# Kernel optimization log

Measured on AMD Instinct MI355X. Metric: run time of the kernel, lower is better.

## Reference

```python
import jax, jax.numpy as jnp
import numpy as np

TOP_K = 2
N_EXP = 64
EVAL_CAPACITY = 2.0


def setup_inputs() -> dict:
    key = jax.random.key(0)
    k1, k2 = jax.random.split(key)
    x = jax.random.normal(k1, (4, 4096, 2048), dtype=jnp.float32)
    w_g = jax.random.normal(k2, (N_EXP, 2048), dtype=jnp.float32) * 0.02  # Linear(n_embd, n_exp, bias=False)
    return {"x": x, "w_g": w_g}


def reference(x, w_g):
    B, T, C = x.shape
    num_tokens = B * T
    x_flat = x.reshape(num_tokens, C)
    # gating logits: [N, E]
    logits = jnp.einsum('nc,ec->ne', x_flat, w_g)
    # top-k selection
    top_k_logits, top_k_indices = jax.lax.top_k(logits, TOP_K)  # [N, k]
    router_probs = jax.nn.softmax(top_k_logits, axis=-1)        # [N, k]
    # static expert capacity (eval path)
    exp_capacity = max(int(TOP_K * EVAL_CAPACITY * num_tokens / N_EXP), 4)
    # one-hot expert mask [N, k, E]
    expert_mask = jax.nn.one_hot(top_k_indices, N_EXP, dtype=jnp.int32)
    # rank tokens within each expert via cumsum over (k-major, token) order
    reshaped = expert_mask.transpose(1, 0, 2).reshape(TOP_K * num_tokens, N_EXP)
    cumsum = jnp.cumsum(reshaped, axis=0)
    position = cumsum.reshape(TOP_K, num_tokens, N_EXP).transpose(1, 0, 2)  # [N, k, E]
    rank = (position - 1) * expert_mask
    capacity_mask = (rank < exp_capacity).astype(jnp.int32)
    final_mask = expert_mask * capacity_mask                     # [N, k, E]
    probs_mask = (final_mask.sum(axis=-1) > 0)                   # [N, k] bool
    router_probs_masked = router_probs * probs_mask.astype(router_probs.dtype)
    final_rank = rank.sum(axis=-1)                               # [N, k]
    return final_mask, router_probs_masked, top_k_indices, final_rank, exp_capacity
```

## Files before the change

kernel.cpp:

```cpp
#include <hip/hip_runtime.h>
#include <math.h>

#define C_DIM 2048
#define E_DIM 64
#define KC    128
#define BT    32
#define NW    4

typedef _Float16 h4    __attribute__((ext_vector_type(4)));
typedef _Float16 v8hf  __attribute__((ext_vector_type(8)));
typedef float    f32x4 __attribute__((ext_vector_type(4)));

#define SCALE      64.0f
#define INV_SCALE2 (1.0f/4096.0f)

__launch_bounds__(256)
__global__ void k_wsplit(const float* __restrict__ w, _Float16* __restrict__ wfrag)
{
    int t  = blockIdx.x * 256 + threadIdx.x;
    int l  = t & 63;
    int ni = (t >> 6) & 3;
    int q  = t >> 8;
    int e  = 16 * ni + (l & 15);
    int k0 = 32 * q + (l >> 4) * 8;
    const float* src = w + (size_t)e * C_DIM + k0;
    float4 a = *(const float4*)(src);
    float4 b = *(const float4*)(src + 4);
    float s[8] = {a.x, a.y, a.z, a.w, b.x, b.y, b.z, b.w};
    v8hf hv, lv;
#pragma unroll
    for (int j = 0; j < 8; ++j) {
        float sc = s[j] * SCALE;
        _Float16 h = (_Float16)sc;
        hv[j] = h;
        lv[j] = (_Float16)(sc - (float)h);
    }
    size_t fo = (size_t)(q * 4 + ni) * 1024;
    *(v8hf*)(wfrag + fo + l * 8)       = hv;
    *(v8hf*)(wfrag + fo + 512 + l * 8) = lv;
}

__launch_bounds__(256)
__global__ void k_logits_top2(const float* __restrict__ x, const _Float16* __restrict__ wfrag,
                              unsigned char* __restrict__ idx0, unsigned char* __restrict__ idx1,
                              float* __restrict__ dlt, unsigned short* __restrict__ gcounts,
                              int nblk)
{
    __shared__ alignas(16) char smem[2 * 16384];

    const int tid  = threadIdx.x;
    const int lane = tid & 63;
    const int wk   = tid >> 6;
    const int ln15 = lane & 15;
    const int g    = lane >> 4;
    const int t0   = blockIdx.x * BT;

    f32x4 acc[2][4];
#pragma unroll
    for (int mi = 0; mi < 2; ++mi)
#pragma unroll
        for (int ni = 0; ni < 4; ++ni) acc[mi][ni] = (f32x4)0.0f;

    float4 xr[4];
    v8hf bh[2][4], bl[2][4];

#define LOADX(kb)                                                               \
    {                                                                           \
        _Pragma("unroll")                                                       \
        for (int r = 0; r < 4; ++r) {                                           \
            int i = tid + 256 * r;                                              \
            int row = i >> 5, c4 = i & 31;                                      \
            xr[r] = *(const float4*)(x + (size_t)(t0 + row) * C_DIM + (kb) + c4 * 4); \
        }                                                                       \
    }

#define STOREX(bf)                                                              \
    {                                                                           \
        _Pragma("unroll")                                                       \
        for (int r = 0; r < 4; ++r) {                                           \
            int i = tid + 256 * r;                                              \
            int row = i >> 5, c4 = i & 31;                                      \
            float4 v = xr[r];                                                   \
            float s0 = v.x * SCALE, s1 = v.y * SCALE, s2 = v.z * SCALE, s3 = v.w * SCALE; \
            _Float16 h0 = (_Float16)s0, h1 = (_Float16)s1, h2 = (_Float16)s2, h3 = (_Float16)s3; \
            h4 hv = {h0, h1, h2, h3};                                           \
            h4 lv = {(_Float16)(s0 - (float)h0), (_Float16)(s1 - (float)h1),    \
                     (_Float16)(s2 - (float)h2), (_Float16)(s3 - (float)h3)};   \
            int boff = (bf) * 16384 + row * 256 + ((c4 * 8) ^ ((row & 7) << 4));\
            *(h4*)(smem + boff)        = hv;                                    \
            *(h4*)(smem + boff + 8192) = lv;                                    \
        }                                                                       \
    }

#define LOADB(c, s)                                                             \
    {                                                                           \
        const char* wp = (const char*)wfrag + ((size_t)(4 * (c) + wk) << 13) + (lane << 4); \
        _Pragma("unroll")                                                       \
        for (int ni = 0; ni < 4; ++ni) {                                        \
            bh[s][ni] = *(const v8hf*)(wp + ni * 2048);                         \
            bl[s][ni] = *(const v8hf*)(wp + ni * 2048 + 1024);                  \
        }                                                                       \
    }

    LOADX(0);
    LOADB(0, 0);
    STOREX(0);
    __syncthreads();

    const int sw   = (ln15 & 7) << 4;
    const int koff = ((wk << 6) + (g << 4)) ^ sw;

#pragma unroll
    for (int c = 0; c < 16; ++c) {
        const int cur = c & 1, nxt = cur ^ 1;
        if (c < 15) {
            LOADX((c + 1) * KC);
            LOADB(c + 1, nxt);
        }
        v8hf ah[2], al[2];
#pragma unroll
        for (int mi = 0; mi < 2; ++mi) {
            int ro = cur * 16384 + (16 * mi + ln15) * 256 + koff;
            ah[mi] = *(const v8hf*)(smem + ro);
            al[mi] = *(const v8hf*)(smem + ro + 8192);
        }
#pragma unroll
        for (int ni = 0; ni < 4; ++ni)
#pragma unroll
            for (int mi = 0; mi < 2; ++mi) {
                acc[mi][ni] = __builtin_amdgcn_mfma_f32_16x16x32_f16(ah[mi], bh[cur][ni], acc[mi][ni], 0, 0, 0);
                acc[mi][ni] = __builtin_amdgcn_mfma_f32_16x16x32_f16(ah[mi], bl[cur][ni], acc[mi][ni], 0, 0, 0);
                acc[mi][ni] = __builtin_amdgcn_mfma_f32_16x16x32_f16(al[mi], bh[cur][ni], acc[mi][ni], 0, 0, 0);
            }
        if (c < 15) STOREX(nxt);
        __syncthreads();
    }

    float* lgs = (float*)smem;
    int*   cnt = (int*)(smem + 8192);
    if (tid < 128) cnt[tid] = 0;
#pragma unroll
    for (int w = 0; w < NW; ++w) {
        if (wk == w) {
#pragma unroll
            for (int mi = 0; mi < 2; ++mi)
#pragma unroll
                for (int ni = 0; ni < 4; ++ni)
#pragma unroll
                    for (int gg = 0; gg < 4; ++gg) {
                        int row = 16 * mi + (g << 2) + gg;
                        int e   = 16 * ni + ln15;
                        float vv = acc[mi][ni][gg] * INV_SCALE2;
                        if (w == 0) lgs[row * 64 + e]  = vv;
                        else        lgs[row * 64 + e] += vv;
                    }
        }
        __syncthreads();
    }

#pragma unroll
    for (int t = 0; t < 8; ++t) {
        int rowl = (wk << 3) + t;
        float v = lgs[rowl * 64 + lane];
        float vv = v; int ix = lane;
#pragma unroll
        for (int off = 32; off > 0; off >>= 1) {
            float ov = __shfl_down(vv, off, 64);
            int   oi = __shfl_down(ix, off, 64);
            if (ov > vv || (ov == vv && oi < ix)) { vv = ov; ix = oi; }
        }
        int   i1 = __shfl(ix, 0, 64);
        float v1 = __shfl(vv, 0, 64);

        vv = (lane == i1) ? -3.0e38f : v; ix = lane;
#pragma unroll
        for (int off = 32; off > 0; off >>= 1) {
            float ov = __shfl_down(vv, off, 64);
            int   oi = __shfl_down(ix, off, 64);
            if (ov > vv || (ov == vv && oi < ix)) { vv = ov; ix = oi; }
        }
        int   i2 = __shfl(ix, 0, 64);
        float v2 = __shfl(vv, 0, 64);

        if (lane == 0) {
            int n = t0 + rowl;
            idx0[n] = (unsigned char)i1;
            idx1[n] = (unsigned char)i2;
            dlt[n]  = v2 - v1;
            atomicAdd(&cnt[i1], 1);
            atomicAdd(&cnt[64 + i2], 1);
        }
    }

    __syncthreads();
    if (tid < 128) {
        int e = tid & 63, k = tid >> 6;
        gcounts[(size_t)e * (2 * nblk) + k * nblk + blockIdx.x] = (unsigned short)cnt[tid];
    }
}

__launch_bounds__(64)
__global__ void k_scan2(unsigned short* __restrict__ g, int S)
{
    const int e = blockIdx.x, lane = threadIdx.x;
    unsigned short* row = g + (size_t)e * S;
    int vals[16];
    const int R = S >> 6;
#pragma unroll
    for (int r = 0; r < 16; ++r) if (r < R) vals[r] = row[(r << 6) + lane];
    int running = 0;
#pragma unroll
    for (int r = 0; r < 16; ++r) {
        if (r >= R) break;
        int v = vals[r], s = v;
#pragma unroll
        for (int off = 1; off < 64; off <<= 1) {
            int t = __shfl_up(s, off, 64);
            if (lane >= off) s += t;
        }
        row[(r << 6) + lane] = (unsigned short)(s - v + running);
        running += __shfl(s, 63, 64);
    }
}

__launch_bounds__(128)
__global__ void k_rank_out(const unsigned char* __restrict__ idx0, const unsigned char* __restrict__ idx1,
                           const unsigned short* __restrict__ gpre, const float* __restrict__ dlt,
                           float* __restrict__ out, int N, int cap, int nblk)
{
    const int b = blockIdx.x, tid = threadIdx.x;
    const int lane = tid & 63, kk = tid >> 6;
    const int t0 = b * BT;
    __shared__ int sm_ix[2][BT], sm_rk[2][BT];

    int v = -1, base = 0;
    if (lane < BT) {
        v = (kk ? idx1 : idx0)[t0 + lane];
        base = gpre[(size_t)v * (2 * nblk) + kk * nblk + b];
    }
    const unsigned long long ltm = (1ull << lane) - 1ull;
    int pre = 0;
    for (int e = 0; e < 64; ++e) {
        unsigned long long bb = __ballot(v == e);
        if (v == e) pre = __popcll(bb & ltm);
    }
    if (lane < BT) { sm_ix[kk][lane] = v; sm_rk[kk][lane] = base + pre; }
    __syncthreads();

#pragma unroll
    for (int rep = 0; rep < 8; ++rep) {
        int f   = tid + 128 * rep;
        int n2  = f >> 5;
        int rem = (f & 31) * 4;
        int kq  = rem >> 6;
        int e0  = rem & 63;
        int ix  = sm_ix[kq][n2];
        int rr  = sm_rk[kq][n2];
        float val = (rr < cap) ? 1.0f : 0.0f;
        float4 o = make_float4(0.f, 0.f, 0.f, 0.f);
        int d = ix - e0;
        if (d >= 0 && d < 4) ((float*)&o)[d] = val;
        *(float4*)(out + (size_t)(t0 + n2) * 128 + rem) = o;
    }

    size_t B = (size_t)2 * N * E_DIM;
    if (tid < 2 * BT) {
        int n2 = tid >> 1, kq = tid & 1;
        int n  = t0 + n2;
        int gi = 2 * n + kq;
        int ix = sm_ix[kq][n2];
        int rr = sm_rk[kq][n2];
        float d  = dlt[n];
        float e1 = expf(d);
        float inv = 1.0f / (1.0f + e1);
        float p  = kq ? (e1 * inv) : inv;
        bool keep = rr < cap;
        out[B + gi]         = keep ? p : 0.0f;
        out[B + 2 * N + gi] = (float)ix;
        out[B + 4 * N + gi] = (float)rr;
    }
    if (b == 0 && tid == 0) out[B + 6 * N] = (float)cap;
}

extern "C" void kernel_launch(void* const* d_in, const int* in_sizes, int n_in,
                              void* d_out, int out_size, void* d_ws, size_t ws_size,
                              hipStream_t stream)
{
    const float* x  = (const float*)d_in[0];
    const float* wg = (const float*)d_in[1];
    const int N = in_sizes[0] / C_DIM;
    const int nblk = N / BT;

    char* ws = (char*)d_ws;
    unsigned char*  idx0    = (unsigned char*)ws;
    unsigned char*  idx1    = idx0 + N;
    float*          dlt     = (float*)(idx1 + N);
    unsigned short* gcounts = (unsigned short*)(dlt + N);
    _Float16*       wfrag   = (_Float16*)(gcounts + (size_t)64 * 2 * nblk);

    float* out = (float*)d_out;

    int cap = (int)((long long)2 * 2 * N / E_DIM);
    if (cap < 4) cap = 4;

    k_wsplit<<<64, 256, 0, stream>>>(wg, wfrag);
    k_logits_top2<<<nblk, 256, 0, stream>>>(x, wfrag, idx0, idx1, dlt, gcounts, nblk);
    k_scan2<<<E_DIM, 64, 0, stream>>>(gcounts, 2 * nblk);
    k_rank_out<<<nblk, 128, 0, stream>>>(idx0, idx1, gcounts, dlt, out, N, cap, nblk);
}
```

Baseline: 240.8 us.

## Load x fragments directly from global into MFMA registers, drop LDS staging

Each wave now reads its x operand fragments straight from global memory into registers in the MFMA lane layout and does the fp16 hi/lo split in registers. This removes the shared-memory double buffer, the swizzled LDS stores and reads, and the per-chunk __syncthreads in the K loop. In exchange, the global loads are 32-byte per-lane strided reads rather than the earlier coalesced ones, and register pressure rises because of the prefetched float4 fragments. Shared memory drops to the logits and count buffers, which may raise occupancy.

Measured after the change: 253.7 us. +5.4%, slower.

```diff
diff --git a/kernel.cpp b/kernel.cpp
--- a/kernel.cpp
+++ b/kernel.cpp
@@ -3,11 +3,9 @@
 
 #define C_DIM 2048
 #define E_DIM 64
-#define KC    128
 #define BT    32
 #define NW    4
 
-typedef _Float16 h4    __attribute__((ext_vector_type(4)));
 typedef _Float16 v8hf  __attribute__((ext_vector_type(8)));
 typedef float    f32x4 __attribute__((ext_vector_type(4)));
 
@@ -46,7 +44,8 @@
                               float* __restrict__ dlt, unsigned short* __restrict__ gcounts,
                               int nblk)
 {
-    __shared__ alignas(16) char smem[2 * 16384];
+    __shared__ float lgs[BT * E_DIM];
+    __shared__ int   cnt[128];
 
     const int tid  = threadIdx.x;
     const int lane = tid & 63;
@@ -55,92 +54,73 @@
     const int g    = lane >> 4;
     const int t0   = blockIdx.x * BT;
 
+    if (tid < 128) cnt[tid] = 0;
+
     f32x4 acc[2][4];
 #pragma unroll
     for (int mi = 0; mi < 2; ++mi)
 #pragma unroll
         for (int ni = 0; ni < 4; ++ni) acc[mi][ni] = (f32x4)0.0f;
 
-    float4 xr[4];
-    v8hf bh[2][4], bl[2][4];
-
-#define LOADX(kb)                                                               \
+    const float* xb = x + (size_t)(t0 + ln15) * C_DIM + 32 * wk + 8 * g;
+    const char*  wb = (const char*)wfrag + ((size_t)wk << 13) + (lane << 4);
+
+    float4 axf[2][2][2];
+    v8hf   bhf[2][4], blf[2][4];
+
+#define LOADSTEP(c, s)                                                          \
     {                                                                           \
         _Pragma("unroll")                                                       \
-        for (int r = 0; r < 4; ++r) {                                           \
-            int i = tid + 256 * r;                                              \
-            int row = i >> 5, c4 = i & 31;                                      \
-            xr[r] = *(const float4*)(x + (size_t)(t0 + row) * C_DIM + (kb) + c4 * 4); \
+        for (int mi = 0; mi < 2; ++mi) {                                        \
+            const float* p = xb + (size_t)(16 * mi) * C_DIM + (c) * 128;        \
+            axf[s][mi][0] = *(const float4*)(p);                                \
+            axf[s][mi][1] = *(const float4*)(p + 4);                            \
         }                                                                       \
-    }
-
-#define STOREX(bf)                                                              \
+        const char* wp = wb + (size_t)(c) * 32768;                              \
+        _Pragma("unroll")                                                       \
+        for (int ni = 0; ni < 4; ++ni) {                                        \
+            bhf[s][ni] = *(const v8hf*)(wp + ni * 2048);                        \
+            blf[s][ni] = *(const v8hf*)(wp + ni * 2048 + 1024);                 \
+        }                                                                       \
+    }
+
+#define DOSTEP(s)                                                               \
     {                                                                           \
-        _Pragma("unroll")                                                       \
-        for (int r = 0; r < 4; ++r) {                                           \
-            int i = tid + 256 * r;                                              \
-            int row = i >> 5, c4 = i & 31;                                      \
-            float4 v = xr[r];                                                   \
-            float s0 = v.x * SCALE, s1 = v.y * SCALE, s2 = v.z * SCALE, s3 = v.w * SCALE; \
-            _Float16 h0 = (_Float16)s0, h1 = (_Float16)s1, h2 = (_Float16)s2, h3 = (_Float16)s3; \
-            h4 hv = {h0, h1, h2, h3};                                           \
-            h4 lv = {(_Float16)(s0 - (float)h0), (_Float16)(s1 - (float)h1),    \
-                     (_Float16)(s2 - (float)h2), (_Float16)(s3 - (float)h3)};   \
-            int boff = (bf) * 16384 + row * 256 + ((c4 * 8) ^ ((row & 7) << 4));\
-            *(h4*)(smem + boff)        = hv;                                    \
-            *(h4*)(smem + boff + 8192) = lv;                                    \
+        v8hf ah[2], al[2];                                                      \
+        _Pragma("unroll")                                                       \
+        for (int mi = 0; mi < 2; ++mi) {                                        \
+            float sv[8] = {axf[s][mi][0].x, axf[s][mi][0].y, axf[s][mi][0].z,   \
+                           axf[s][mi][0].w, axf[s][mi][1].x, axf[s][mi][1].y,   \
+                           axf[s][mi][1].z, axf[s][mi][1].w};                   \
+            _Pragma("unroll")                                                   \
+            for (int j = 0; j < 8; ++j) {                                       \
+                float sc = sv[j] * SCALE;                                       \
+                _Float16 h = (_Float16)sc;                                      \
+                ah[mi][j] = h;                                                  \
+                al[mi][j] = (_Float16)(sc - (float)h);                          \
+            }                                                                   \
         }                                                                       \
-    }
-
-#define LOADB(c, s)                                                             \
-    {                                                                           \
-        const char* wp = (const char*)wfrag + ((size_t)(4 * (c) + wk) << 13) + (lane << 4); \
-        _Pragma("unroll")                                                       \
-        for (int ni = 0; ni < 4; ++ni) {                                        \
-            bh[s][ni] = *(const v8hf*)(wp + ni * 2048);                         \
-            bl[s][ni] = *(const v8hf*)(wp + ni * 2048 + 1024);                  \
-        }                                                                       \
-    }
-
-    LOADX(0);
-    LOADB(0, 0);
-    STOREX(0);
-    __syncthreads();
-
-    const int sw   = (ln15 & 7) << 4;
-    const int koff = ((wk << 6) + (g << 4)) ^ sw;
-
+        _Pragma("unroll")                                                       \
+        for (int ni = 0; ni < 4; ++ni)                                          \
+            _Pragma("unroll")                                                   \
+            for (int mi = 0; mi < 2; ++mi) {                                    \
+                acc[mi][ni] = __builtin_amdgcn_mfma_f32_16x16x32_f16(ah[mi], bhf[s][ni], acc[mi][ni], 0, 0, 0); \
+                acc[mi][ni] = __builtin_amdgcn_mfma_f32_16x16x32_f16(ah[mi], blf[s][ni], acc[mi][ni], 0, 0, 0); \
+                acc[mi][ni] = __builtin_amdgcn_mfma_f32_16x16x32_f16(al[mi], bhf[s][ni], acc[mi][ni], 0, 0, 0); \
+            }                                                                   \
+    }
+
+    LOADSTEP(0, 0);
 #pragma unroll
     for (int c = 0; c < 16; ++c) {
-        const int cur = c & 1, nxt = cur ^ 1;
-        if (c < 15) {
-            LOADX((c + 1) * KC);
-            LOADB(c + 1, nxt);
-        }
-        v8hf ah[2], al[2];
-#pragma unroll
-        for (int mi = 0; mi < 2; ++mi) {
-            int ro = cur * 16384 + (16 * mi + ln15) * 256 + koff;
-            ah[mi] = *(const v8hf*)(smem + ro);
-            al[mi] = *(const v8hf*)(smem + ro + 8192);
-        }
-#pragma unroll
-        for (int ni = 0; ni < 4; ++ni)
-#pragma unroll
-            for (int mi = 0; mi < 2; ++mi) {
-                acc[mi][ni] = __builtin_amdgcn_mfma_f32_16x16x32_f16(ah[mi], bh[cur][ni], acc[mi][ni], 0, 0, 0);
-                acc[mi][ni] = __builtin_amdgcn_mfma_f32_16x16x32_f16(ah[mi], bl[cur][ni], acc[mi][ni], 0, 0, 0);
-                acc[mi][ni] = __builtin_amdgcn_mfma_f32_16x16x32_f16(al[mi], bh[cur][ni], acc[mi][ni], 0, 0, 0);
-            }
-        if (c < 15) STOREX(nxt);
-        __syncthreads();
-    }
-
-    float* lgs = (float*)smem;
-    int*   cnt = (int*)(smem + 8192);
-    if (tid < 128) cnt[tid] = 0;
+        const int cur = c & 1;
+        if (c < 15) LOADSTEP(c + 1, cur ^ 1);
+        DOSTEP(cur);
+    }
+
 #pragma unroll
     for (int w = 0; w < NW; ++w) {
+        if (w > 0) __syncthreads();
         if (wk == w) {
 #pragma unroll
             for (int mi = 0; mi < 2; ++mi)
@@ -155,8 +135,8 @@
                         else        lgs[row * 64 + e] += vv;
                     }
         }
-        __syncthreads();
-    }
+    }
+    __syncthreads();
 
 #pragma unroll
     for (int t = 0; t < 8; ++t) {
```
